# Performance work log

Measured on AMD Instinct MI355X. Metric: run time of the kernel, lower is better.

The kernel has to match this reference:

```python
import jax, jax.numpy as jnp
import numpy as np

NUM_HEADS = 12
D_MODEL = 768


def setup_inputs() -> dict:
    key = jax.random.key(0)
    ks = jax.random.split(key, 5)
    B, S = 2, 2048
    x = jax.random.normal(ks[0], (B, S, D_MODEL), dtype=jnp.float32)
    # additive causal mask: 0 on/below diagonal, -1e9 above
    causal = jnp.tril(jnp.ones((S, S), dtype=bool))
    attn_mask = jnp.where(causal, 0.0, -1e9).astype(jnp.float32)
    lim_in = 1.0 / np.sqrt(D_MODEL)
    w_in = jax.random.uniform(ks[1], (3 * D_MODEL, D_MODEL), jnp.float32, -lim_in, lim_in)
    b_in = jax.random.uniform(ks[2], (3 * D_MODEL,), jnp.float32, -lim_in, lim_in)
    w_out = jax.random.uniform(ks[3], (D_MODEL, D_MODEL), jnp.float32, -lim_in, lim_in)
    b_out = jax.random.uniform(ks[4], (D_MODEL,), jnp.float32, -lim_in, lim_in)
    return {"x": x, "attn_mask": attn_mask, "w_in": w_in, "b_in": b_in,
            "w_out": w_out, "b_out": b_out}


def reference(x, attn_mask, w_in, b_in, w_out, b_out):
    B, S, d_model = x.shape
    H = NUM_HEADS
    d_head = d_model // H
    # fused QKV projection (torch Linear: x @ W^T + b)
    projected = x @ w_in.T + b_in                      # [B, S, 3*d_model]
    # faithful reinterpretation as in the source: row-major view to
    # [B*H, S, d_head, 3] (q/k/v interleaved on last axis, heads folded
    # across the flat buffer). No 1/sqrt(d_head) scaling in the source.
    qkv = projected.reshape(B * H, S, d_head, 3)
    q = qkv[..., 0]                                    # [B*H, S, d_head]
    k = qkv[..., 1]
    v = qkv[..., 2]
    logits = jnp.einsum('nsd,ntd->nst', q, k) + attn_mask  # [B*H, S, S]
    weights = jax.nn.softmax(logits, axis=-1)          # dropout_p = 0
    heads = jnp.einsum('nst,ntd->nsd', weights, v)     # [B*H, S, d_head]
    out = heads.reshape(B, H, S, d_head).transpose(0, 2, 1, 3).reshape(B, S, d_model)
    return out @ w_out.T + b_out
```

## Files before the change

kernel.cpp:

```cpp
#include <hip/hip_runtime.h>
#include <hip/hip_bf16.h>
#include <stdint.h>

typedef __attribute__((ext_vector_type(8))) short bf16x8;
typedef __attribute__((ext_vector_type(4))) float f32x4;
typedef __attribute__((ext_vector_type(16))) float f32x16;
typedef __attribute__((ext_vector_type(4))) unsigned short u16x4;

__device__ __forceinline__ unsigned short f2bf(float f) {
    unsigned int u = __builtin_bit_cast(unsigned int, f);
    u = (u + 0x7fffu + ((u >> 16) & 1u)) >> 16;
    return (unsigned short)u;
}

__device__ __forceinline__ void gl2lds16(const void* g, void* l) {
    __builtin_amdgcn_global_load_lds(
        (const __attribute__((address_space(1))) unsigned int*)g,
        (__attribute__((address_space(3))) unsigned int*)l, 16, 0, 0);
}

__global__ __launch_bounds__(256)
void cvt_all(const float* __restrict__ x, const float* __restrict__ wi, const float* __restrict__ wo,
             unsigned short* __restrict__ xb, unsigned short* __restrict__ wb1,
             unsigned short* __restrict__ wb2) {
    const int bid = blockIdx.x;
    const float* src; unsigned short* dst; int i;
    if (bid < 3072)      { src = x;  dst = xb;  i = bid * 256 + threadIdx.x; }
    else if (bid < 4800) { src = wi; dst = wb1; i = (bid - 3072) * 256 + threadIdx.x; }
    else                 { src = wo; dst = wb2; i = (bid - 4800) * 256 + threadIdx.x; }
    float4 v = reinterpret_cast<const float4*>(src)[i];
    union { unsigned short u[4]; uint2 p; } o;
    o.u[0] = f2bf(v.x); o.u[1] = f2bf(v.y); o.u[2] = f2bf(v.z); o.u[3] = f2bf(v.w);
    reinterpret_cast<uint2*>(dst)[i] = o.p;
}

template<int BM, int BN>
__global__ __launch_bounds__(256)
void gemm_bt(const unsigned short* __restrict__ A, const unsigned short* __restrict__ B,
             const float* __restrict__ bias, int M, int N, int K, int mode,
             unsigned short* __restrict__ bf_out, float* __restrict__ f32_out) {
    __shared__ unsigned short Al[2][BM][32];
    __shared__ unsigned short Bl[2][BN][32];
    const int tid = threadIdx.x;
    const int wid = tid >> 6, lane = tid & 63;
    const int m0 = blockIdx.y * BM, n0 = blockIdx.x * BN;
    const int wm = (wid >> 1) * (BM / 2), wn = (wid & 1) * (BN / 2);
    const int lrow = lane & 15;
    constexpr int MR = BM / 32, NR = BN / 32;
    f32x4 acc[MR][NR];
#pragma unroll
    for (int a = 0; a < MR; a++)
#pragma unroll
        for (int b = 0; b < NR; b++) acc[a][b] = f32x4{0.f, 0.f, 0.f, 0.f};

    auto stage = [&](int buf, int k0) {
#pragma unroll
        for (int i = 0; i < BM / 64; i++) {
            const int fb = i * 256 + tid;
            const int row = fb >> 2, blk = fb & 3;
            const int sb = blk ^ ((row >> 1) & 3);
            gl2lds16(&A[(size_t)(m0 + row) * K + k0 + sb * 8],
                     (char*)&Al[buf][0][0] + (i * 256 + (tid & ~63)) * 16);
        }
#pragma unroll
        for (int i = 0; i < BN / 64; i++) {
            const int fb = i * 256 + tid;
            const int row = fb >> 2, blk = fb & 3;
            const int sb = blk ^ ((row >> 1) & 3);
            gl2lds16(&B[(size_t)(n0 + row) * K + k0 + sb * 8],
                     (char*)&Bl[buf][0][0] + (i * 256 + (tid & ~63)) * 16);
        }
    };

    stage(0, 0);
    const int NS = K >> 5;
    for (int it = 0; it < NS; ++it) {
        __syncthreads();
        const int cur = it & 1;
        if (it + 1 < NS) stage(cur ^ 1, (it + 1) << 5);
        bf16x8 af[MR], bfr[NR];
#pragma unroll
        for (int i = 0; i < MR; i++) {
            const int row = wm + i * 16 + lrow;
            const int g = (lane >> 4) ^ ((row >> 1) & 3);
            af[i] = *reinterpret_cast<const bf16x8*>(&Al[cur][row][g * 8]);
        }
#pragma unroll
        for (int i = 0; i < NR; i++) {
            const int row = wn + i * 16 + lrow;
            const int g = (lane >> 4) ^ ((row >> 1) & 3);
            bfr[i] = *reinterpret_cast<const bf16x8*>(&Bl[cur][row][g * 8]);
        }
#pragma unroll
        for (int mi = 0; mi < MR; mi++)
#pragma unroll
            for (int ni = 0; ni < NR; ni++)
                acc[mi][ni] = __builtin_amdgcn_mfma_f32_16x16x32_bf16(af[mi], bfr[ni], acc[mi][ni], 0, 0, 0);
    }
    const int rb = (lane >> 4) * 4;
#pragma unroll
    for (int mi = 0; mi < MR; mi++)
#pragma unroll
        for (int ni = 0; ni < NR; ni++) {
            int cc = n0 + wn + ni * 16 + lrow;
            float bv = bias[cc];
#pragma unroll
            for (int i = 0; i < 4; i++) {
                int r = m0 + wm + mi * 16 + rb + i;
                float v = acc[mi][ni][i] + bv;
                if (mode == 0) {
                    bf_out[(size_t)r * N + cc] = f2bf(v);
                } else {
                    f32_out[(size_t)r * N + cc] = v;
                }
            }
        }
}

__global__ __launch_bounds__(256)
void deint(const unsigned short* __restrict__ P, unsigned short* __restrict__ qkv,
           unsigned int* __restrict__ ctr) {
    __shared__ unsigned short L[6144];
    const int tid = threadIdx.x;
    if (blockIdx.x == 0 && tid == 0) *ctr = 0u;
    const size_t base = (size_t)blockIdx.x * 6144;
#pragma unroll
    for (int s = 0; s < 3; ++s) {
        int idx = (s * 256 + tid) * 8;
        *reinterpret_cast<bf16x8*>(&L[idx]) = *reinterpret_cast<const bf16x8*>(&P[base + idx]);
    }
    __syncthreads();
    const int u0 = blockIdx.x * 32;
    const int n = u0 >> 11, t0 = u0 & 2047;
#pragma unroll
    for (int s = 0; s < 2; ++s) {
        int ww = s * 256 + tid;
        int j = ww >> 8;
        int cc = (ww & 255) >> 3;
        int o = ww & 7;
        bf16x8 vv;
#pragma unroll
        for (int q = 0; q < 8; ++q) vv[q] = (short)L[cc * 192 + 3 * (o * 8 + q) + j];
        *reinterpret_cast<bf16x8*>(&qkv[(size_t)j * 3145728 + (size_t)(u0 + cc) * 64 + o * 8]) = vv;
    }
    {
        int d = tid >> 2, g = tid & 3;
        bf16x8 vv;
#pragma unroll
        for (int e = 0; e < 8; ++e) vv[e] = (short)L[(g * 8 + e) * 192 + 3 * d + 2];
        *reinterpret_cast<bf16x8*>(&qkv[6291456 + (size_t)n * 131072 + (size_t)d * 2048 + t0 + g * 8]) = vv;
    }
}

#define ANITEMS 960
__global__ __launch_bounds__(256, 2)
void attn_fwd(const unsigned short* __restrict__ qkv, unsigned short* __restrict__ Hb,
              float* __restrict__ Op, float2* __restrict__ Ml, unsigned int* __restrict__ ctr) {
    __shared__ unsigned short Kl[2][64][64];
    __shared__ unsigned short Vl[2][64][64];
    __shared__ int s_item;
    static const unsigned char CLS[40] = {
        60,61,62,63, 56,57,58, 52,53,54, 48,49,50, 44,45,46, 40,41, 36,37,
        32,33, 28,29, 24, 20, 16, 12, 59,42,25,8, 55,38,21,4, 51,34,17,0};
    const int tid = threadIdx.x, w = tid >> 6, lane = tid & 63;
    const int l31 = lane & 31, l7 = lane & 7, hi = lane >> 5;

    for (;;) {
        __syncthreads();
        if (tid == 0) s_item = (int)atomicAdd(ctr, 1u);
        __syncthreads();
        const int item = s_item;
        if (item >= ANITEMS) break;
        const int c = item / 24;
        const int n = item - c * 24;
        const int v = CLS[c];
        const int qb = v >> 2, ch = v & 3;
        const int ntfull = 2 * qb + 2;
        const int nch = (ntfull + 7) >> 3;
        const int split = (nch > 1) ? 1 : 0;
        const int tstart = ch * 8;
        const int nt = (ntfull - tstart < 8) ? (ntfull - tstart) : 8;
        const int q0w = qb * 128 + w * 32;
        const int q_lane = q0w + l31;
        const unsigned short* Qg = qkv + (size_t)n * 131072;
        const unsigned short* Kg = qkv + 3145728 + (size_t)n * 131072;
        const unsigned short* Vg = qkv + 6291456 + (size_t)n * 131072;

        bf16x8 qf[4];
#pragma unroll
        for (int s = 0; s < 4; s++)
            qf[s] = *reinterpret_cast<const bf16x8*>(&Qg[(size_t)q_lane * 64 + 16*s + 8*hi]);

        f32x16 oa[2];
#pragma unroll
        for (int dt = 0; dt < 2; dt++)
#pragma unroll
            for (int r = 0; r < 16; r++) oa[dt][r] = 0.f;
        float m_run = -3.0e38f, l_run = 0.f;

        auto stage = [&](int buf, int gt) {
            const int tb = gt * 64;
#pragma unroll
            for (int i = 0; i < 2; i++) {
                const int fb_base = i * 256 + (tid & ~63);
                const int fb = i * 256 + tid;
                const int t = fb >> 3, p = fb & 7;
                gl2lds16(&Kg[(size_t)(tb + t) * 64 + ((p ^ (t & 7)) << 3)],
                         (char*)&Kl[buf][0][0] + fb_base * 16);
                gl2lds16(&Vg[(size_t)t * 2048 + tb + ((p ^ (t & 7)) << 3)],
                         (char*)&Vl[buf][0][0] + fb_base * 16);
            }
        };

        stage(0, tstart);
        int cur = 0;
        for (int tt = 0; tt < nt; ++tt) {
            __syncthreads();
            const int t0 = (tstart + tt) * 64;
            if (tt + 1 < nt) stage(cur ^ 1, tstart + tt + 1);
            if (t0 <= q0w + 31) {
                f32x16 sa[2];
#pragma unroll
                for (int t2 = 0; t2 < 2; t2++)
#pragma unroll
                    for (int r = 0; r < 16; r++) sa[t2][r] = 0.f;
#pragma unroll
                for (int t2 = 0; t2 < 2; t2++)
#pragma unroll
                    for (int s = 0; s < 4; s++) {
                        bf16x8 kf = *reinterpret_cast<const bf16x8*>(
                            &Kl[cur][32*t2 + l31][((2*s + hi) ^ l7) << 3]);
                        sa[t2] = __builtin_amdgcn_mfma_f32_32x32x16_bf16(kf, qf[s], sa[t2], 0, 0, 0);
                    }
                if (t0 + 63 > q0w) {
#pragma unroll
                    for (int t2 = 0; t2 < 2; t2++)
#pragma unroll
                        for (int r = 0; r < 16; r++) {
                            int t = t0 + 32*t2 + (r & 3) + 8*(r >> 2) + 4*hi;
                            if (t > q_lane) sa[t2][r] = -1e30f;
                        }
                }
                float mx = sa[0][0];
#pragma unroll
                for (int t2 = 0; t2 < 2; t2++)
#pragma unroll
                    for (int r = 0; r < 16; r++) mx = fmaxf(mx, sa[t2][r]);
                mx = fmaxf(mx, __shfl_xor(mx, 32));
                float mn = fmaxf(m_run, mx);
                float alpha = __expf(m_run - mn);
                m_run = mn;
                float rs = 0.f;
#pragma unroll
                for (int t2 = 0; t2 < 2; t2++)
#pragma unroll
                    for (int r = 0; r < 16; r++) {
                        float p = __expf(sa[t2][r] - mn);
                        sa[t2][r] = p;
                        rs += p;
                    }
                rs += __shfl_xor(rs, 32);
                l_run = l_run * alpha + rs;
#pragma unroll
                for (int dt = 0; dt < 2; dt++)
#pragma unroll
                    for (int r = 0; r < 16; r++) oa[dt][r] *= alpha;
                bf16x8 pfrag[4];
#pragma unroll
                for (int t2 = 0; t2 < 2; t2++) {
                    unsigned int pk[8];
#pragma unroll
                    for (int k2 = 0; k2 < 8; k2++) {
                        float lo = sa[t2][2*k2], hi2 = sa[t2][2*k2 + 1];
                        unsigned int r;
                        asm("v_cvt_pk_bf16_f32 %0, %1, %2" : "=v"(r) : "v"(lo), "v"(hi2));
                        pk[k2] = r;
                    }
                    asm("v_permlane32_swap_b32 %0, %1" : "+v"(pk[0]), "+v"(pk[2]));
                    asm("v_permlane32_swap_b32 %0, %1" : "+v"(pk[1]), "+v"(pk[3]));
                    asm("v_permlane32_swap_b32 %0, %1" : "+v"(pk[4]), "+v"(pk[6]));
                    asm("v_permlane32_swap_b32 %0, %1" : "+v"(pk[5]), "+v"(pk[7]));
                    union { unsigned int u[4]; bf16x8 v; } f0, f1;
                    f0.u[0] = pk[0]; f0.u[1] = pk[1]; f0.u[2] = pk[2]; f0.u[3] = pk[3];
                    f1.u[0] = pk[4]; f1.u[1] = pk[5]; f1.u[2] = pk[6]; f1.u[3] = pk[7];
                    pfrag[2*t2]     = f0.v;
                    pfrag[2*t2 + 1] = f1.v;
                }
#pragma unroll
                for (int dt = 0; dt < 2; dt++)
#pragma unroll
                    for (int sp = 0; sp < 4; sp++) {
                        bf16x8 vf = *reinterpret_cast<const bf16x8*>(
                            &Vl[cur][32*dt + l31][((2*sp + hi) ^ l7) << 3]);
                        oa[dt] = __builtin_amdgcn_mfma_f32_32x32x16_bf16(vf, pfrag[sp], oa[dt], 0, 0, 0);
                    }
            }
            cur ^= 1;
        }
        const int b = n / 12, h = n - (n / 12) * 12;
        if (!split) {
            const float inv = 1.0f / l_run;
            const size_t rowb = ((size_t)(b * 2048 + q_lane)) * 768 + h * 64;
#pragma unroll
            for (int dt = 0; dt < 2; dt++)
#pragma unroll
                for (int g = 0; g < 4; g++) {
                    u16x4 o4;
#pragma unroll
                    for (int e = 0; e < 4; e++) o4[e] = f2bf(oa[dt][4*g + e] * inv);
                    *reinterpret_cast<u16x4*>(&Hb[rowb + 32*dt + 8*g + 4*hi]) = o4;
                }
        } else {
            const int rr = q_lane - 512;
            const size_t pbase = ((size_t)(n * 1536 + rr) * 4 + ch) * 64;
#pragma unroll
            for (int dt = 0; dt < 2; dt++)
#pragma unroll
                for (int g = 0; g < 4; g++) {
                    float4 o4;
                    o4.x = oa[dt][4*g + 0]; o4.y = oa[dt][4*g + 1];
                    o4.z = oa[dt][4*g + 2]; o4.w = oa[dt][4*g + 3];
                    *reinterpret_cast<float4*>(&Op[pbase + 32*dt + 8*g + 4*hi]) = o4;
                }
            if (hi == 0) {
                float2 mlv; mlv.x = m_run; mlv.y = l_run;
                Ml[(n * 1536 + rr) * 4 + ch] = mlv;
            }
        }
    }
}

__global__ __launch_bounds__(256)
void attn_combine(const float* __restrict__ Op, const float2* __restrict__ Ml,
                  unsigned short* __restrict__ Hb) {
    const int idx = blockIdx.x * 256 + threadIdx.x;
    const int d = idx & 63, rowg = idx >> 6;
    const int n = rowg / 1536, rr = rowg - n * 1536;
    const int qb = (512 + rr) >> 7;
    const int nch = (2 * qb + 9) >> 3;
    float M = -3.0e38f;
    for (int c = 0; c < nch; c++) M = fmaxf(M, Ml[rowg * 4 + c].x);
    float lsum = 0.f, osum = 0.f;
    for (int c = 0; c < nch; c++) {
        const float2 ml = Ml[rowg * 4 + c];
        const float wgt = __expf(ml.x - M);
        lsum += wgt * ml.y;
        osum += wgt * Op[(size_t)(rowg * 4 + c) * 64 + d];
    }
    const int bb = n / 12, h = n - (n / 12) * 12;
    Hb[((size_t)(bb * 2048 + 512 + rr)) * 768 + h * 64 + d] = f2bf(osum / lsum);
}

extern "C" void kernel_launch(void* const* d_in, const int* in_sizes, int n_in,
                              void* d_out, int out_size, void* d_ws, size_t ws_size,
                              hipStream_t stream) {
    const float* x     = (const float*)d_in[0];
    const float* w_in  = (const float*)d_in[2];
    const float* b_in  = (const float*)d_in[3];
    const float* w_out = (const float*)d_in[4];
    const float* b_out = (const float*)d_in[5];
    float* out = (float*)d_out;

    unsigned short* xb   = (unsigned short*)d_ws;
    unsigned short* wb1  = xb  + 3145728;
    unsigned short* wb2  = wb1 + 1769472;
    unsigned short* proj = wb2 + 589824;
    unsigned short* qkvb = proj + 9437184;
    unsigned short* hb   = qkvb + 9437184;
    float*        Op  = (float*)(hb + 3145728);
    float2*       Ml  = (float2*)(Op + 9437184);
    unsigned int* ctr = (unsigned int*)xb;

    cvt_all<<<5376, 256, 0, stream>>>(x, w_in, w_out, xb, wb1, wb2);

    gemm_bt<128,128><<<dim3(18, 32), 256, 0, stream>>>(
        xb, wb1, b_in, 4096, 2304, 768, 0, proj, nullptr);

    deint<<<1536, 256, 0, stream>>>(proj, qkvb, ctr);

    attn_fwd<<<512, 256, 0, stream>>>(qkvb, hb, Op, Ml, ctr);

    attn_combine<<<9216, 256, 0, stream>>>(Op, Ml, hb);

    gemm_bt<128,64><<<dim3(12, 32), 256, 0, stream>>>(
        hb, wb2, b_out, 4096, 768, 768, 1, nullptr, out);
}
```

Measured before the change: 186.6 us.

## Use static grid with lazy softmax rescale and bf16 partials in attention

Replaces the atomic-counter persistent work loop with one block per work item (960 blocks) and raises the launch bound to 4 blocks per CU. It also adds a lazy online-softmax rescale that only updates the running max when it grows by more than 8, sets wave priority around the MFMA sections, and stores split partial outputs as bf16 instead of fp32 to halve combine traffic. These target scheduling overhead, exp/rescale work, and partial-output bandwidth, at the cost of extra register pressure under the tighter occupancy bound and slightly lower precision in the partials.

```diff
diff --git a/kernel.cpp b/kernel.cpp
--- a/kernel.cpp
+++ b/kernel.cpp
@@ -11,6 +11,11 @@
     unsigned int u = __builtin_bit_cast(unsigned int, f);
     u = (u + 0x7fffu + ((u >> 16) & 1u)) >> 16;
     return (unsigned short)u;
+}
+
+__device__ __forceinline__ float bf2f(unsigned short u) {
+    unsigned int x = ((unsigned int)u) << 16;
+    return __builtin_bit_cast(float, x);
 }
 
 __device__ __forceinline__ void gl2lds16(const void* g, void* l) {
@@ -118,11 +123,9 @@
 }
 
 __global__ __launch_bounds__(256)
-void deint(const unsigned short* __restrict__ P, unsigned short* __restrict__ qkv,
-           unsigned int* __restrict__ ctr) {
+void deint(const unsigned short* __restrict__ P, unsigned short* __restrict__ qkv) {
     __shared__ unsigned short L[6144];
     const int tid = threadIdx.x;
-    if (blockIdx.x == 0 && tid == 0) *ctr = 0u;
     const size_t base = (size_t)blockIdx.x * 6144;
 #pragma unroll
     for (int s = 0; s < 3; ++s) {
@@ -152,186 +155,185 @@
     }
 }
 
-#define ANITEMS 960
-__global__ __launch_bounds__(256, 2)
+__global__ __launch_bounds__(256, 4)
 void attn_fwd(const unsigned short* __restrict__ qkv, unsigned short* __restrict__ Hb,
-              float* __restrict__ Op, float2* __restrict__ Ml, unsigned int* __restrict__ ctr) {
+              unsigned short* __restrict__ Op, float2* __restrict__ Ml) {
     __shared__ unsigned short Kl[2][64][64];
     __shared__ unsigned short Vl[2][64][64];
-    __shared__ int s_item;
     static const unsigned char CLS[40] = {
         60,61,62,63, 56,57,58, 52,53,54, 48,49,50, 44,45,46, 40,41, 36,37,
         32,33, 28,29, 24, 20, 16, 12, 59,42,25,8, 55,38,21,4, 51,34,17,0};
     const int tid = threadIdx.x, w = tid >> 6, lane = tid & 63;
     const int l31 = lane & 31, l7 = lane & 7, hi = lane >> 5;
 
-    for (;;) {
+    const int item = blockIdx.x;
+    const int c = item / 24;
+    const int n = item - c * 24;
+    const int v = CLS[c];
+    const int qb = v >> 2, ch = v & 3;
+    const int ntfull = 2 * qb + 2;
+    const int nch = (ntfull + 7) >> 3;
+    const int split = (nch > 1) ? 1 : 0;
+    const int tstart = ch * 8;
+    const int nt = (ntfull - tstart < 8) ? (ntfull - tstart) : 8;
+    const int q0w = qb * 128 + w * 32;
+    const int q_lane = q0w + l31;
+    const unsigned short* Qg = qkv + (size_t)n * 131072;
+    const unsigned short* Kg = qkv + 3145728 + (size_t)n * 131072;
+    const unsigned short* Vg = qkv + 6291456 + (size_t)n * 131072;
+
+    bf16x8 qf[4];
+#pragma unroll
+    for (int s = 0; s < 4; s++)
+        qf[s] = *reinterpret_cast<const bf16x8*>(&Qg[(size_t)q_lane * 64 + 16*s + 8*hi]);
+
+    f32x16 oa[2];
+#pragma unroll
+    for (int dt = 0; dt < 2; dt++)
+#pragma unroll
+        for (int r = 0; r < 16; r++) oa[dt][r] = 0.f;
+    float m_run = -3.0e38f, l_run = 0.f;
+
+    auto stage = [&](int buf, int gt) {
+        const int tb = gt * 64;
+#pragma unroll
+        for (int i = 0; i < 2; i++) {
+            const int fb_base = i * 256 + (tid & ~63);
+            const int fb = i * 256 + tid;
+            const int t = fb >> 3, p = fb & 7;
+            gl2lds16(&Kg[(size_t)(tb + t) * 64 + ((p ^ (t & 7)) << 3)],
+                     (char*)&Kl[buf][0][0] + fb_base * 16);
+            gl2lds16(&Vg[(size_t)t * 2048 + tb + ((p ^ (t & 7)) << 3)],
+                     (char*)&Vl[buf][0][0] + fb_base * 16);
+        }
+    };
+
+    stage(0, tstart);
+    int cur = 0;
+    for (int tt = 0; tt < nt; ++tt) {
         __syncthreads();
-        if (tid == 0) s_item = (int)atomicAdd(ctr, 1u);
-        __syncthreads();
-        const int item = s_item;
-        if (item >= ANITEMS) break;
-        const int c = item / 24;
-        const int n = item - c * 24;
-        const int v = CLS[c];
-        const int qb = v >> 2, ch = v & 3;
-        const int ntfull = 2 * qb + 2;
-        const int nch = (ntfull + 7) >> 3;
-        const int split = (nch > 1) ? 1 : 0;
-        const int tstart = ch * 8;
-        const int nt = (ntfull - tstart < 8) ? (ntfull - tstart) : 8;
-        const int q0w = qb * 128 + w * 32;
-        const int q_lane = q0w + l31;
-        const unsigned short* Qg = qkv + (size_t)n * 131072;
-        const unsigned short* Kg = qkv + 3145728 + (size_t)n * 131072;
-        const unsigned short* Vg = qkv + 6291456 + (size_t)n * 131072;
-
-        bf16x8 qf[4];
-#pragma unroll
-        for (int s = 0; s < 4; s++)
-            qf[s] = *reinterpret_cast<const bf16x8*>(&Qg[(size_t)q_lane * 64 + 16*s + 8*hi]);
-
-        f32x16 oa[2];
+        const int t0 = (tstart + tt) * 64;
+        if (tt + 1 < nt) stage(cur ^ 1, tstart + tt + 1);
+        if (t0 <= q0w + 31) {
+            f32x16 sa[2];
+#pragma unroll
+            for (int t2 = 0; t2 < 2; t2++)
+#pragma unroll
+                for (int r = 0; r < 16; r++) sa[t2][r] = 0.f;
+            __builtin_amdgcn_s_setprio(1);
+#pragma unroll
+            for (int t2 = 0; t2 < 2; t2++)
+#pragma unroll
+                for (int s = 0; s < 4; s++) {
+                    bf16x8 kf = *reinterpret_cast<const bf16x8*>(
+                        &Kl[cur][32*t2 + l31][((2*s + hi) ^ l7) << 3]);
+                    sa[t2] = __builtin_amdgcn_mfma_f32_32x32x16_bf16(kf, qf[s], sa[t2], 0, 0, 0);
+                }
+            __builtin_amdgcn_s_setprio(0);
+            if (t0 + 63 > q0w) {
+#pragma unroll
+                for (int t2 = 0; t2 < 2; t2++)
+#pragma unroll
+                    for (int r = 0; r < 16; r++) {
+                        int t = t0 + 32*t2 + (r & 3) + 8*(r >> 2) + 4*hi;
+                        if (t > q_lane) sa[t2][r] = -1e30f;
+                    }
+            }
+            float pm = sa[0][0];
+#pragma unroll
+            for (int t2 = 0; t2 < 2; t2++)
+#pragma unroll
+                for (int r = 0; r < 16; r++) pm = fmaxf(pm, sa[t2][r]);
+            pm = fmaxf(pm, __shfl_xor(pm, 32));
+            if (__any(pm > m_run + 8.f)) {
+                float mn = fmaxf(m_run, pm);
+                float alpha = __expf(m_run - mn);
+                l_run *= alpha;
+#pragma unroll
+                for (int dt = 0; dt < 2; dt++)
+#pragma unroll
+                    for (int r = 0; r < 16; r++) oa[dt][r] *= alpha;
+                m_run = mn;
+            }
+            float rs = 0.f;
+#pragma unroll
+            for (int t2 = 0; t2 < 2; t2++)
+#pragma unroll
+                for (int r = 0; r < 16; r++) {
+                    float p = __expf(sa[t2][r] - m_run);
+                    sa[t2][r] = p;
+                    rs += p;
+                }
+            rs += __shfl_xor(rs, 32);
+            l_run += rs;
+            bf16x8 pfrag[4];
+#pragma unroll
+            for (int t2 = 0; t2 < 2; t2++) {
+                unsigned int pk[8];
+#pragma unroll
+                for (int k2 = 0; k2 < 8; k2++) {
+                    float lo = sa[t2][2*k2], hi2 = sa[t2][2*k2 + 1];
+                    unsigned int r;
+                    asm("v_cvt_pk_bf16_f32 %0, %1, %2" : "=v"(r) : "v"(lo), "v"(hi2));
+                    pk[k2] = r;
+                }
+                asm("v_permlane32_swap_b32 %0, %1" : "+v"(pk[0]), "+v"(pk[2]));
+                asm("v_permlane32_swap_b32 %0, %1" : "+v"(pk[1]), "+v"(pk[3]));
+                asm("v_permlane32_swap_b32 %0, %1" : "+v"(pk[4]), "+v"(pk[6]));
+                asm("v_permlane32_swap_b32 %0, %1" : "+v"(pk[5]), "+v"(pk[7]));
+                union { unsigned int u[4]; bf16x8 v; } f0, f1;
+                f0.u[0] = pk[0]; f0.u[1] = pk[1]; f0.u[2] = pk[2]; f0.u[3] = pk[3];
+                f1.u[0] = pk[4]; f1.u[1] = pk[5]; f1.u[2] = pk[6]; f1.u[3] = pk[7];
+                pfrag[2*t2]     = f0.v;
+                pfrag[2*t2 + 1] = f1.v;
+            }
+            __builtin_amdgcn_s_setprio(1);
+#pragma unroll
+            for (int dt = 0; dt < 2; dt++)
+#pragma unroll
+                for (int sp = 0; sp < 4; sp++) {
+                    bf16x8 vf = *reinterpret_cast<const bf16x8*>(
+                        &Vl[cur][32*dt + l31][((2*sp + hi) ^ l7) << 3]);
+                    oa[dt] = __builtin_amdgcn_mfma_f32_32x32x16_bf16(vf, pfrag[sp], oa[dt], 0, 0, 0);
+                }
+            __builtin_amdgcn_s_setprio(0);
+        }
+        cur ^= 1;
+    }
+    const int b = n / 12, h = n - (n / 12) * 12;
+    if (!split) {
+        const float inv = 1.0f / l_run;
+        const size_t rowb = ((size_t)(b * 2048 + q_lane)) * 768 + h * 64;
 #pragma unroll
         for (int dt = 0; dt < 2; dt++)
 #pragma unroll
-            for (int r = 0; r < 16; r++) oa[dt][r] = 0.f;
-        float m_run = -3.0e38f, l_run = 0.f;
-
-        auto stage = [&](int buf, int gt) {
-            const int tb = gt * 64;
-#pragma unroll
-            for (int i = 0; i < 2; i++) {
-                const int fb_base = i * 256 + (tid & ~63);
-                const int fb = i * 256 + tid;
-                const int t = fb >> 3, p = fb & 7;
-                gl2lds16(&Kg[(size_t)(tb + t) * 64 + ((p ^ (t & 7)) << 3)],
-                         (char*)&Kl[buf][0][0] + fb_base * 16);
-                gl2lds16(&Vg[(size_t)t * 2048 + tb + ((p ^ (t & 7)) << 3)],
-                         (char*)&Vl[buf][0][0] + fb_base * 16);
-            }
-        };
-
-        stage(0, tstart);
-        int cur = 0;
-        for (int tt = 0; tt < nt; ++tt) {
-            __syncthreads();
-            const int t0 = (tstart + tt) * 64;
-            if (tt + 1 < nt) stage(cur ^ 1, tstart + tt + 1);
-            if (t0 <= q0w + 31) {
-                f32x16 sa[2];
-#pragma unroll
-                for (int t2 = 0; t2 < 2; t2++)
-#pragma unroll
-                    for (int r = 0; r < 16; r++) sa[t2][r] = 0.f;
-#pragma unroll
-                for (int t2 = 0; t2 < 2; t2++)
-#pragma unroll
-                    for (int s = 0; s < 4; s++) {
-                        bf16x8 kf = *reinterpret_cast<const bf16x8*>(
-                            &Kl[cur][32*t2 + l31][((2*s + hi) ^ l7) << 3]);
-                        sa[t2] = __builtin_amdgcn_mfma_f32_32x32x16_bf16(kf, qf[s], sa[t2], 0, 0, 0);
-                    }
-                if (t0 + 63 > q0w) {
-#pragma unroll
-                    for (int t2 = 0; t2 < 2; t2++)
-#pragma unroll
-                        for (int r = 0; r < 16; r++) {
-                            int t = t0 + 32*t2 + (r & 3) + 8*(r >> 2) + 4*hi;
-                            if (t > q_lane) sa[t2][r] = -1e30f;
-                        }
-                }
-                float mx = sa[0][0];
-#pragma unroll
-                for (int t2 = 0; t2 < 2; t2++)
-#pragma unroll
-                    for (int r = 0; r < 16; r++) mx = fmaxf(mx, sa[t2][r]);
-                mx = fmaxf(mx, __shfl_xor(mx, 32));
-                float mn = fmaxf(m_run, mx);
-                float alpha = __expf(m_run - mn);
-                m_run = mn;
-                float rs = 0.f;
-#pragma unroll
-                for (int t2 = 0; t2 < 2; t2++)
-#pragma unroll
-                    for (int r = 0; r < 16; r++) {
-                        float p = __expf(sa[t2][r] - mn);
-                        sa[t2][r] = p;
-                        rs += p;
-                    }
-                rs += __shfl_xor(rs, 32);
-                l_run = l_run * alpha + rs;
-#pragma unroll
-                for (int dt = 0; dt < 2; dt++)
-#pragma unroll
-                    for (int r = 0; r < 16; r++) oa[dt][r] *= alpha;
-                bf16x8 pfrag[4];
-#pragma unroll
-                for (int t2 = 0; t2 < 2; t2++) {
-                    unsigned int pk[8];
-#pragma unroll
-                    for (int k2 = 0; k2 < 8; k2++) {
-                        float lo = sa[t2][2*k2], hi2 = sa[t2][2*k2 + 1];
-                        unsigned int r;
-                        asm("v_cvt_pk_bf16_f32 %0, %1, %2" : "=v"(r) : "v"(lo), "v"(hi2));
-                        pk[k2] = r;
-                    }
-                    asm("v_permlane32_swap_b32 %0, %1" : "+v"(pk[0]), "+v"(pk[2]));
-                    asm("v_permlane32_swap_b32 %0, %1" : "+v"(pk[1]), "+v"(pk[3]));
-                    asm("v_permlane32_swap_b32 %0, %1" : "+v"(pk[4]), "+v"(pk[6]));
-                    asm("v_permlane32_swap_b32 %0, %1" : "+v"(pk[5]), "+v"(pk[7]));
-                    union { unsigned int u[4]; bf16x8 v; } f0, f1;
-                    f0.u[0] = pk[0]; f0.u[1] = pk[1]; f0.u[2] = pk[2]; f0.u[3] = pk[3];
-                    f1.u[0] = pk[4]; f1.u[1] = pk[5]; f1.u[2] = pk[6]; f1.u[3] = pk[7];
-                    pfrag[2*t2]     = f0.v;
-                    pfrag[2*t2 + 1] = f1.v;
-                }
-#pragma unroll
-                for (int dt = 0; dt < 2; dt++)
-#pragma unroll
-                    for (int sp = 0; sp < 4; sp++) {
-                        bf16x8 vf = *reinterpret_cast<const bf16x8*>(
-                            &Vl[cur][32*dt + l31][((2*sp + hi) ^ l7) << 3]);
-                        oa[dt] = __builtin_amdgcn_mfma_f32_32x32x16_bf16(vf, pfrag[sp], oa[dt], 0, 0, 0);
-                    }
-            }
-            cur ^= 1;
-        }
-        const int b = n / 12, h = n - (n / 12) * 12;
-        if (!split) {
-            const float inv = 1.0f / l_run;
-            const size_t rowb = ((size_t)(b * 2048 + q_lane)) * 768 + h * 64;
-#pragma unroll
-            for (int dt = 0; dt < 2; dt++)
-#pragma unroll
-                for (int g = 0; g < 4; g++) {
-                    u16x4 o4;
-#pragma unroll
-                    for (int e = 0; e < 4; e++) o4[e] = f2bf(oa[dt][4*g + e] * inv);
-                    *reinterpret_cast<u16x4*>(&Hb[rowb + 32*dt + 8*g + 4*hi]) = o4;
-                }
-        } else {
-            const int rr = q_lane - 512;
-            const size_t pbase = ((size_t)(n * 1536 + rr) * 4 + ch) * 64;
-#pragma unroll
-            for (int dt = 0; dt < 2; dt++)
-#pragma unroll
-                for (int g = 0; g < 4; g++) {
-                    float4 o4;
-                    o4.x = oa[dt][4*g + 0]; o4.y = oa[dt][4*g + 1];
-                    o4.z = oa[dt][4*g + 2]; o4.w = oa[dt][4*g + 3];
-                    *reinterpret_cast<float4*>(&Op[pbase + 32*dt + 8*g + 4*hi]) = o4;
-                }
-            if (hi == 0) {
-                float2 mlv; mlv.x = m_run; mlv.y = l_run;
-                Ml[(n * 1536 + rr) * 4 + ch] = mlv;
-            }
+            for (int g = 0; g < 4; g++) {
+                u16x4 o4;
+#pragma unroll
+                for (int e = 0; e < 4; e++) o4[e] = f2bf(oa[dt][4*g + e] * inv);
+                *reinterpret_cast<u16x4*>(&Hb[rowb + 32*dt + 8*g + 4*hi]) = o4;
+            }
+    } else {
+        const int rr = q_lane - 512;
+        const size_t pbase = ((size_t)(n * 1536 + rr) * 4 + ch) * 64;
+#pragma unroll
+        for (int dt = 0; dt < 2; dt++)
+#pragma unroll
+            for (int g = 0; g < 4; g++) {
+                u16x4 o4;
+#pragma unroll
+                for (int e = 0; e < 4; e++) o4[e] = f2bf(oa[dt][4*g + e]);
+                *reinterpret_cast<u16x4*>(&Op[pbase + 32*dt + 8*g + 4*hi]) = o4;
+            }
+        if (hi == 0) {
+            float2 mlv; mlv.x = m_run; mlv.y = l_run;
+            Ml[(n * 1536 + rr) * 4 + ch] = mlv;
         }
     }
 }
 
 __global__ __launch_bounds__(256)
-void attn_combine(const float* __restrict__ Op, const float2* __restrict__ Ml,
+void attn_combine(const unsigned short* __restrict__ Op, const float2* __restrict__ Ml,
                   unsigned short* __restrict__ Hb) {
     const int idx = blockIdx.x * 256 + threadIdx.x;
     const int d = idx & 63, rowg = idx >> 6;
@@ -345,7 +347,7 @@
         const float2 ml = Ml[rowg * 4 + c];
         const float wgt = __expf(ml.x - M);
         lsum += wgt * ml.y;
-        osum += wgt * Op[(size_t)(rowg * 4 + c) * 64 + d];
+        osum += wgt * bf2f(Op[(size_t)(rowg * 4 + c) * 64 + d]);
     }
     const int bb = n / 12, h = n - (n / 12) * 12;
     Hb[((size_t)(bb * 2048 + 512 + rr)) * 768 + h * 64 + d] = f2bf(osum / lsum);
@@ -367,20 +369,19 @@
     unsigned short* proj = wb2 + 589824;
     unsigned short* qkvb = proj + 9437184;
     unsigned short* hb   = qkvb + 9437184;
-    float*        Op  = (float*)(hb + 3145728);
-    float2*       Ml  = (float2*)(Op + 9437184);
-    unsigned int* ctr = (unsigned int*)xb;
+    unsigned short* Opb  = hb + 3145728;
+    float2*       Ml  = (float2*)(Opb + 9437184);
 
     cvt_all<<<5376, 256, 0, stream>>>(x, w_in, w_out, xb, wb1, wb2);
 
     gemm_bt<128,128><<<dim3(18, 32), 256, 0, stream>>>(
         xb, wb1, b_in, 4096, 2304, 768, 0, proj, nullptr);
 
-    deint<<<1536, 256, 0, stream>>>(proj, qkvb, ctr);
-
-    attn_fwd<<<512, 256, 0, stream>>>(qkvb, hb, Op, Ml, ctr);
-
-    attn_combine<<<9216, 256, 0, stream>>>(Op, Ml, hb);
+    deint<<<1536, 256, 0, stream>>>(proj, qkvb);
+
+    attn_fwd<<<960, 256, 0, stream>>>(qkvb, hb, Opb, Ml);
+
+    attn_combine<<<9216, 256, 0, stream>>>(Opb, Ml, hb);
 
     gemm_bt<128,64><<<dim3(12, 32), 256, 0, stream>>>(
         hb, wb2, b_out, 4096, 768, 768, 1, nullptr, out);
```

After: 173.2 us. 1.08x faster.
